# Performance work log

Measured on AMD Instinct MI355X. Metric: run time of the kernel, lower is better.

Reference implementation:

```python
import jax, jax.numpy as jnp
import numpy as np

D = 768        # d_model
F = 8192       # dict_size
N_UP = 3       # number of upstream autoencoders
K = 64         # topk
B, S = 2, 1024


def setup_inputs() -> dict:
    key = jax.random.key(0)
    ks = jax.random.split(key, 10)
    sc = 1.0 / np.sqrt(D)
    return {
        "feature_buffer": jnp.zeros((B, S, F), jnp.float32),
        "x": jax.random.normal(ks[0], (B, S, D), jnp.float32),
        "up_feats": jax.random.uniform(ks[1], (N_UP, B, S, F), jnp.float32),
        "W_enc": jax.random.normal(ks[2], (D, F), jnp.float32) * sc,
        "b_enc": jax.random.normal(ks[3], (F,), jnp.float32) * 0.01,
        "W_dec": jax.random.normal(ks[4], (F, D), jnp.float32) * sc,
        "b_dec": jax.random.normal(ks[5], (D,), jnp.float32) * 0.01,
        "up_W_dec": jax.random.normal(ks[6], (N_UP, F, D), jnp.float32) * sc,
        "up_b_dec": jax.random.normal(ks[7], (N_UP, D), jnp.float32) * 0.01,
        "conn_mask": jax.random.randint(ks[8], (N_UP, F, F), 0, 2).astype(bool),
        "k": K,
    }


def reference(feature_buffer, x, up_feats, W_enc, b_enc, W_dec, b_dec,
              up_W_dec, up_b_dec, conn_mask, k):
    # initial contribs: residual stream through current encoder
    approx = jnp.einsum("bsd,df->bsf", x, W_enc)            # [B,S,F]
    upstream_bias = jnp.zeros((D,), x.dtype)
    # accumulate pruned contributions from each upstream AE
    for i in range(up_feats.shape[0]):
        upstream_bias = upstream_bias + up_b_dec[i]
        # virtual weights up_dict -> down_dict, pruned by connection mask
        virt = (up_W_dec[i] @ W_enc) * conn_mask[i].astype(x.dtype)  # [F_up,F_down]
        approx = approx + jnp.einsum("bsf,fg->bsg", up_feats[i], virt)
    # bias correction: upstream decoder biases through encoder, plus encoder bias
    approx = approx + upstream_bias @ W_enc + b_enc          # [B,S,F]
    # topk + relu + scatter into the feature buffer
    top_vals, top_idx = jax.lax.top_k(approx, k)             # [B,S,k]
    top_vals = jax.nn.relu(top_vals)
    flat = feature_buffer.reshape(-1, F)
    rows = jnp.arange(flat.shape[0])[:, None]
    feat = flat.at[rows, top_idx.reshape(-1, k)].set(top_vals.reshape(-1, k))
    feat = feat.reshape(feature_buffer.shape)
    # decode
    return jnp.einsum("bsf,fd->bsd", feat, W_dec) + b_dec
```

## Files before the change

kernel.cpp:

```cpp
#include <hip/hip_runtime.h>
#include <hip/hip_bf16.h>


#define D_DIM 768
#define F_DIM 8192

typedef _Float16 f16;
typedef _Float16 f16x8 __attribute__((ext_vector_type(8)));
typedef float f32x4 __attribute__((ext_vector_type(4)));

#define BMN 128
#define BUFB 32768
#define PLNB 16384

__device__ inline void split_f32(float v, f16& h, f16& l) {
    float hf = (float)(f16)v;
    if (__builtin_fabsf(hf) < 6.1035156e-5f) hf = 0.f;
    h = (f16)hf;
    l = (f16)((v - hf) * 2048.0f);
}

template<int MODE>
__global__ __launch_bounds__(256, 2)
void mfma_gemm(const f16* __restrict__ Ap,
               const f16* __restrict__ Bp,
               float* __restrict__ C, int ldc,
               f16* __restrict__ Vp,
               const float* __restrict__ bias,
               const unsigned char* __restrict__ conn, int upIdx,
               const int* __restrict__ flagp,
               int K, int fdBase)
{
    __shared__ char lds[2 * BUFB];
    const int tid = threadIdx.x;
    const int bm = (MODE == 2 ? blockIdx.x : blockIdx.y) * BMN;
    const int bn = (MODE == 2 ? blockIdx.y : blockIdx.x) * BMN;

    const int w  = tid >> 6;
    const int l  = tid & 63;
    const int wr = (w >> 1) * 64;
    const int wc = (w & 1) * 64;

    const char* gsrc[8];
    #pragma unroll
    for (int j = 0; j < 8; ++j) {
        const int c = tid + 256 * j;
        const int p = c >> 10;
        const int q = c & 1023;
        const int r = q >> 3;
        const int sp = q & 7;
        const int slog = sp ^ (r & 7);
        const f16* base = p ? Bp : Ap;
        const int row0 = p ? bn : bm;
        gsrc[j] = (const char*)base + (size_t)(row0 + r) * ((size_t)K * 4)
                  + slog * 16;
    }

    #define STAGE(BUFSEL)                                                     \
        _Pragma("unroll")                                                     \
        for (int j = 0; j < 8; ++j) {                                         \
            __builtin_amdgcn_global_load_lds(                                 \
                (const __attribute__((address_space(1))) void*)gsrc[j],       \
                (__attribute__((address_space(3))) void*)                     \
                    (lds + (BUFSEL) * BUFB + (tid + 256 * j) * 16),           \
                16, 0, 0);                                                    \
            gsrc[j] += 128;                       \
        }

    f32x4 accH[4][4], accM[4][4];
    const f32x4 zero = {0.f, 0.f, 0.f, 0.f};
    #pragma unroll
    for (int a = 0; a < 4; ++a)
        #pragma unroll
        for (int b = 0; b < 4; ++b) { accH[a][b] = zero; accM[a][b] = zero; }

    const int steps = K >> 5;
    const int fr = l & 15;
    const int ks = l >> 4;

    int offAH[4], offBH[4], offAL[4], offBL[4];
    #pragma unroll
    for (int f = 0; f < 4; ++f) {
        const int ra = wr + f * 16 + fr;
        const int rb = wc + f * 16 + fr;
        offAH[f] = ra * 128 + ((ks ^ (ra & 7)) * 16);
        offAL[f] = ra * 128 + (((4 + ks) ^ (ra & 7)) * 16);
        offBH[f] = PLNB + rb * 128 + ((ks ^ (rb & 7)) * 16);
        offBL[f] = PLNB + rb * 128 + (((4 + ks) ^ (rb & 7)) * 16);
    }

    STAGE(0);
    int cur = 0;
    for (int t = 0; t < steps; ++t) {
        asm volatile("s_waitcnt vmcnt(0)" ::: "memory");
        __syncthreads();

        const char* Lb = lds + cur * BUFB;
        f16x8 ah[4], bh[4];
        #pragma unroll
        for (int mf = 0; mf < 4; ++mf) ah[mf] = *(const f16x8*)(Lb + offAH[mf]);
        #pragma unroll
        for (int nf = 0; nf < 4; ++nf) bh[nf] = *(const f16x8*)(Lb + offBH[nf]);

        if (t + 1 < steps) STAGE(cur ^ 1);

        f16x8 al[4], bl[4];
        #pragma unroll
        for (int nf = 0; nf < 4; ++nf) bl[nf] = *(const f16x8*)(Lb + offBL[nf]);
        #pragma unroll
        for (int mf = 0; mf < 4; ++mf) al[mf] = *(const f16x8*)(Lb + offAL[mf]);

        __builtin_amdgcn_s_setprio(1);
        #pragma unroll
        for (int nf = 0; nf < 4; ++nf)
            #pragma unroll
            for (int mf = 0; mf < 4; ++mf)
                accH[mf][nf] = __builtin_amdgcn_mfma_f32_16x16x32_f16(
                    ah[mf], bh[nf], accH[mf][nf], 0, 0, 0);
        __builtin_amdgcn_s_setprio(0);

        __builtin_amdgcn_s_setprio(1);
        #pragma unroll
        for (int nf = 0; nf < 4; ++nf)
            #pragma unroll
            for (int mf = 0; mf < 4; ++mf)
                accM[mf][nf] = __builtin_amdgcn_mfma_f32_16x16x32_f16(
                    ah[mf], bl[nf], accM[mf][nf], 0, 0, 0);
        #pragma unroll
        for (int mf = 0; mf < 4; ++mf)
            #pragma unroll
            for (int nf = 0; nf < 4; ++nf)
                accM[mf][nf] = __builtin_amdgcn_mfma_f32_16x16x32_f16(
                    al[mf], bh[nf], accM[mf][nf], 0, 0, 0);
        __builtin_amdgcn_s_setprio(0);

        cur ^= 1;
    }
    #undef STAGE

    const float MS = 4.8828125e-4f;
    const int flag = (MODE == 1) ? *flagp : 0;

    #pragma unroll
    for (int mf = 0; mf < 4; ++mf) {
        const int row0 = wr + mf * 16 + (l >> 4) * 4;
        #pragma unroll
        for (int nf = 0; nf < 4; ++nf) {
            const int col = wc + nf * 16 + (l & 15);
            float v[4];
            #pragma unroll
            for (int rr = 0; rr < 4; ++rr)
                v[rr] = accH[mf][nf][rr] + accM[mf][nf][rr] * MS;

            if (MODE == 0) {
                const float bb = bias[bn + col];
                #pragma unroll
                for (int rr = 0; rr < 4; ++rr)
                    C[(size_t)(bm + row0 + rr) * ldc + (bn + col)] = v[rr] + bb;
            } else if (MODE == 2) {
                #pragma unroll
                for (int rr = 0; rr < 4; ++rr) {
                    float* cp = &C[(size_t)(bm + row0 + rr) * ldc + (bn + col)];
                    *cp = *cp + v[rr];
                }
            } else {
                const size_t fu = (size_t)(bn + col);
                const size_t fd0 = (size_t)(fdBase + bm + row0);
                int m[4];
                if (flag == 1) {
                    const int4 mm = *(const int4*)((const int*)conn +
                        (size_t)upIdx * F_DIM * F_DIM + fu * F_DIM + fd0);
                    m[0] = mm.x; m[1] = mm.y; m[2] = mm.z; m[3] = mm.w;
                } else if (flag == 0) {
                    const uchar4 mm = *(const uchar4*)(conn +
                        (size_t)upIdx * F_DIM * F_DIM + fu * F_DIM + fd0);
                    m[0] = mm.x; m[1] = mm.y; m[2] = mm.z; m[3] = mm.w;
                } else if (flag == 2) {
                    const long long* pp = (const long long*)conn +
                        (size_t)upIdx * F_DIM * F_DIM + fu * F_DIM + fd0;
                    m[0] = (int)pp[0]; m[1] = (int)pp[1];
                    m[2] = (int)pp[2]; m[3] = (int)pp[3];
                } else {
                    const float4 mm = *(const float4*)((const float*)conn +
                        (size_t)upIdx * F_DIM * F_DIM + fu * F_DIM + fd0);
                    m[0] = mm.x != 0.f; m[1] = mm.y != 0.f;
                    m[2] = mm.z != 0.f; m[3] = mm.w != 0.f;
                }
                const size_t kblk = (fu >> 5) * 64 + (fu & 31);
                #pragma unroll
                for (int rr = 0; rr < 4; ++rr) {
                    const float vv = m[rr] ? v[rr] : 0.f;
                    f16 hh, ll;
                    split_f32(vv, hh, ll);
                    const size_t o = (size_t)(bm + row0 + rr) * (2 * F_DIM) + kblk;
                    Vp[o] = hh; Vp[o + 32] = ll;
                }
            }
        }
    }
}

__global__ __launch_bounds__(256)
void split_kernel(const float* __restrict__ src, f16* __restrict__ dst,
                  size_t n, int K)
{
    const size_t e = ((size_t)blockIdx.x * 256 + threadIdx.x) * 8;
    if (e >= n) return;
    const size_t r = e / (size_t)K;
    const int k = (int)(e - r * (size_t)K);
    const float4 a = *(const float4*)(src + e);
    const float4 b = *(const float4*)(src + e + 4);
    f16 hv[8], lv[8];
    const float s[8] = {a.x, a.y, a.z, a.w, b.x, b.y, b.z, b.w};
    #pragma unroll
    for (int i = 0; i < 8; ++i) split_f32(s[i], hv[i], lv[i]);
    const size_t base = r * (size_t)(2 * K) + (size_t)((k >> 5) * 64 + (k & 31));
    *(f16x8*)(dst + base)      = *(const f16x8*)hv;
    *(f16x8*)(dst + base + 32) = *(const f16x8*)lv;
}

__global__ __launch_bounds__(256)
void transpose_split_kernel(const float* __restrict__ W, f16* __restrict__ dst)
{
    const int f = blockIdx.x * 256 + threadIdx.x;
    for (int dc = 0; dc < D_DIM / 8; ++dc) {
        const int k = dc * 8;
        f16 hv[8], lv[8];
        #pragma unroll
        for (int j = 0; j < 8; ++j)
            split_f32(W[(size_t)(k + j) * F_DIM + f], hv[j], lv[j]);
        const size_t base = (size_t)f * (2 * D_DIM) + (k >> 5) * 64 + (k & 31);
        *(f16x8*)(dst + base)      = *(const f16x8*)hv;
        *(f16x8*)(dst + base + 32) = *(const f16x8*)lv;
    }
}

__global__ void detect_kernel(const int* __restrict__ conn, int* __restrict__ flag)
{
    __shared__ int not01, notf01, odd_nz;
    if (threadIdx.x == 0) { not01 = 0; notf01 = 0; odd_nz = 0; }
    __syncthreads();
    const int4 v = ((const int4*)conn)[threadIdx.x];
    const unsigned a[4] = {(unsigned)v.x, (unsigned)v.y,
                           (unsigned)v.z, (unsigned)v.w};
    int l_not01 = 0, l_notf = 0;
    #pragma unroll
    for (int i = 0; i < 4; ++i) {
        if (a[i] > 1u) l_not01 = 1;
        if (a[i] != 0u && a[i] != 0x3F800000u) l_notf = 1;
    }
    if (l_not01) atomicOr(&not01, 1);
    if (l_notf)  atomicOr(&notf01, 1);
    if (a[1] | a[3]) atomicOr(&odd_nz, 1);
    __syncthreads();
    if (threadIdx.x == 0) {
        int f;
        if (!not01)        f = odd_nz ? 1 : 2;
        else if (!notf01)  f = 3;
        else               f = 0;
        *flag = f;
    }
}

__global__ void bias2_kernel(const float* __restrict__ W_enc,
                             const float* __restrict__ b_enc,
                             const float* __restrict__ up_b_dec,
                             int nup, float* __restrict__ bias2)
{
    const int g = blockIdx.x * 256 + threadIdx.x;
    if (g >= F_DIM) return;
    float s = b_enc[g];
    for (int d = 0; d < D_DIM; ++d) {
        float ub = 0.f;
        for (int i = 0; i < nup; ++i) ub += up_b_dec[i * D_DIM + d];
        s = __builtin_fmaf(ub, W_enc[(size_t)d * F_DIM + g], s);
    }
    bias2[g] = s;
}

__global__ __launch_bounds__(256)
void topk_decode_kernel(const float* __restrict__ approx,
                        const float* __restrict__ W_dec,
                        const float* __restrict__ b_dec,
                        const int* __restrict__ kptr,
                        float* __restrict__ out)
{
    __shared__ unsigned keys[F_DIM];
    __shared__ int hist[256];
    __shared__ unsigned sh_prefix;
    __shared__ int sh_need;
    __shared__ int sel_cnt, eq_cnt;
    __shared__ int sidx[128];
    __shared__ float sval[128];
    __shared__ int eqidx[1024];

    const int tid = threadIdx.x;
    const int row = blockIdx.x;
    const int k = *kptr;
    const float* arow = approx + (size_t)row * F_DIM;

    for (int j = tid; j < F_DIM; j += 256) {
        unsigned u = __float_as_uint(arow[j]);
        u = (u & 0x80000000u) ? ~u : (u | 0x80000000u);
        keys[j] = u;
    }
    if (tid == 0) { sh_prefix = 0u; sh_need = k; sel_cnt = 0; eq_cnt = 0; }
    __syncthreads();

    for (int shift = 24; shift >= 0; shift -= 8) {
        if (tid < 256) hist[tid] = 0;
        __syncthreads();
        const unsigned pfx = sh_prefix;
        for (int j = tid; j < F_DIM; j += 256) {
            const unsigned u = keys[j];
            const bool match =
                (shift == 24) || ((u >> (shift + 8)) == (pfx >> (shift + 8)));
            if (match) atomicAdd(&hist[(u >> shift) & 255], 1);
        }
        __syncthreads();
        if (tid == 0) {
            int need = sh_need;
            for (int b = 255; b >= 0; --b) {
                const int c = hist[b];
                if (c >= need) {
                    sh_prefix = pfx | ((unsigned)b << shift);
                    sh_need = need;
                    break;
                }
                need -= c;
            }
        }
        __syncthreads();
    }
    const unsigned T = sh_prefix;
    const int r = sh_need;

    for (int j = tid; j < F_DIM; j += 256) {
        const unsigned u = keys[j];
        if (u > T) {
            const int p = atomicAdd(&sel_cnt, 1);
            sidx[p] = j;
        } else if (u == T) {
            const int p = atomicAdd(&eq_cnt, 1);
            if (p < 1024) eqidx[p] = j;
        }
    }
    __syncthreads();

    if (tid == 0) {
        const int m = sel_cnt;
        const int e = eq_cnt < 1024 ? eq_cnt : 1024;
        for (int t2 = 0; t2 < r; ++t2) {
            int best = 0x7FFFFFFF, bi = -1;
            for (int q = 0; q < e; ++q) {
                const int v = eqidx[q];
                if (v >= 0 && v < best) { best = v; bi = q; }
            }
            if (bi >= 0) { eqidx[bi] = -1; sidx[m + t2] = best; }
        }
        sel_cnt = m + r;
        const int n = sel_cnt;
        for (int a2 = 1; a2 < n; ++a2) {
            const int v = sidx[a2];
            int b2 = a2 - 1;
            while (b2 >= 0 && sidx[b2] > v) { sidx[b2 + 1] = sidx[b2]; --b2; }
            sidx[b2 + 1] = v;
        }
    }
    __syncthreads();

    const int total = sel_cnt;
    for (int j = tid; j < total; j += 256) {
        const float v = arow[sidx[j]];
        sval[j] = v > 0.f ? v : 0.f;
    }
    __syncthreads();

    float acc0 = b_dec[tid];
    float acc1 = b_dec[tid + 256];
    float acc2 = b_dec[tid + 512];
    for (int j = 0; j < total; ++j) {
        const float v = sval[j];
        const float* wv = W_dec + (size_t)sidx[j] * D_DIM;
        acc0 = __builtin_fmaf(v, wv[tid],       acc0);
        acc1 = __builtin_fmaf(v, wv[tid + 256], acc1);
        acc2 = __builtin_fmaf(v, wv[tid + 512], acc2);
    }
    float* orow = out + (size_t)row * D_DIM;
    orow[tid] = acc0;
    orow[tid + 256] = acc1;
    orow[tid + 512] = acc2;
}

extern "C" void kernel_launch(void* const* d_in, const int* in_sizes, int n_in,
                              void* d_out, int out_size, void* d_ws, size_t ws_size,
                              hipStream_t stream)
{
    const float* x         = (const float*)d_in[1];
    const float* up_feats  = (const float*)d_in[2];
    const float* W_enc     = (const float*)d_in[3];
    const float* b_enc     = (const float*)d_in[4];
    const float* W_dec     = (const float*)d_in[5];
    const float* b_dec     = (const float*)d_in[6];
    const float* up_W_dec  = (const float*)d_in[7];
    const float* up_b_dec  = (const float*)d_in[8];
    const unsigned char* conn = (const unsigned char*)d_in[9];
    const int* kptr        = (const int*)d_in[10];

    const int BS  = in_sizes[1] / D_DIM;
    const int NUP = in_sizes[8] / D_DIM;

    char* ws = (char*)d_ws;
    size_t off = 0;
    auto alloc = [&](size_t bytes) -> char* {
        off = (off + 255) & ~(size_t)255;
        char* p = ws + off; off += bytes; return p;
    };
    float* approx = (float*)alloc((size_t)BS * F_DIM * 4);
    float* bias2  = (float*)alloc(F_DIM * 4);
    int*   flag   = (int*)alloc(256);
    f16* xp   = (f16*)alloc((size_t)BS * D_DIM * 4);
    f16* Wtp  = (f16*)alloc((size_t)F_DIM * D_DIM * 4);
    f16* uwdp = (f16*)alloc((size_t)NUP * F_DIM * D_DIM * 4);
    f16* ufp  = (f16*)alloc((size_t)NUP * BS * F_DIM * 4);

    off = (off + 255) & ~(size_t)255;
    const size_t rem = (ws_size > off) ? ws_size - off : 0;
    int FC = (int)((rem / ((size_t)F_DIM * 4)) / 128 * 128);
    if (FC > F_DIM) FC = F_DIM;
    if (FC < 128) FC = 128;
    f16* vp = (f16*)alloc((size_t)FC * F_DIM * 4);

    detect_kernel<<<1, 256, 0, stream>>>((const int*)conn, flag);
    bias2_kernel<<<F_DIM / 256, 256, 0, stream>>>(W_enc, b_enc, up_b_dec, NUP, bias2);

    split_kernel<<<(unsigned)((size_t)BS * D_DIM / 2048), 256, 0, stream>>>(
        x, xp, (size_t)BS * D_DIM, D_DIM);
    split_kernel<<<(unsigned)((size_t)NUP * F_DIM * D_DIM / 2048), 256, 0, stream>>>(
        up_W_dec, uwdp, (size_t)NUP * F_DIM * D_DIM, D_DIM);
    split_kernel<<<(unsigned)((size_t)NUP * BS * F_DIM / 2048), 256, 0, stream>>>(
        up_feats, ufp, (size_t)NUP * BS * F_DIM, F_DIM);
    transpose_split_kernel<<<F_DIM / 256, 256, 0, stream>>>(W_enc, Wtp);

    mfma_gemm<0><<<dim3(F_DIM / BMN, BS / BMN), 256, 0, stream>>>(
        xp, Wtp, approx, F_DIM, nullptr, bias2,
        nullptr, 0, flag, D_DIM, 0);

    for (int i = 0; i < NUP; ++i) {
        for (int fc = 0; fc < F_DIM; fc += FC) {
            const int chunk = (F_DIM - fc) < FC ? (F_DIM - fc) : FC;
            mfma_gemm<1><<<dim3(F_DIM / BMN, chunk / BMN), 256, 0, stream>>>(
                Wtp + (size_t)fc * (2 * D_DIM),
                uwdp + (size_t)i * F_DIM * (2 * D_DIM),
                nullptr, 0, vp, nullptr,
                conn, i, flag, D_DIM, fc);
            mfma_gemm<2><<<dim3(BS / BMN, chunk / BMN), 256, 0, stream>>>(
                ufp + (size_t)i * BS * (2 * F_DIM),
                vp,
                approx + fc, F_DIM, nullptr, nullptr,
                nullptr, 0, flag, F_DIM, 0);
        }
    }

    topk_decode_kernel<<<BS, 256, 0, stream>>>(
        approx, W_dec, b_dec, kptr, (float*)d_out);
}
```

Baseline: 3.798 ms.

## Batch virtual-weight GEMMs and fuse all accumulation GEMMs into one segmented K loop

The per-upstream, per-chunk loop of virtual-weight and accumulation GEMM launches is replaced. One launch now computes the masked virtual weights for all upstream AEs, and a single segmented-K GEMM accumulates x·W_enc and the three up_feats·virt products in registers before writing approx once. This removes the repeated read-modify-write of approx and many kernel launches. In exchange it needs a full NUP×F×F split-f16 workspace (about 800 MB) instead of the workspace-sized chunking, and there is a risk of overrunning ws_size.

```diff
diff --git a/kernel.cpp b/kernel.cpp
--- a/kernel.cpp
+++ b/kernel.cpp
@@ -12,6 +12,14 @@
 #define BMN 128
 #define BUFB 32768
 #define PLNB 16384
+
+struct SegDesc {
+    const f16 *a0, *a1, *a2, *a3;
+    const f16 *b0, *b1, *b2, *b3;
+    int str0, str1, str2, str3;
+    int steps0, steps1, steps2, steps3;
+    int totalSteps;
+};
 
 __device__ inline void split_f32(float v, f16& h, f16& l) {
     float hf = (float)(f16)v;
@@ -22,39 +30,54 @@
 
 template<int MODE>
 __global__ __launch_bounds__(256, 2)
-void mfma_gemm(const f16* __restrict__ Ap,
-               const f16* __restrict__ Bp,
-               float* __restrict__ C, int ldc,
+void mfma_gemm(SegDesc d, float* __restrict__ C, int ldc,
                f16* __restrict__ Vp,
                const float* __restrict__ bias,
-               const unsigned char* __restrict__ conn, int upIdx,
-               const int* __restrict__ flagp,
-               int K, int fdBase)
+               const unsigned char* __restrict__ conn,
+               const int* __restrict__ flagp)
 {
     __shared__ char lds[2 * BUFB];
     const int tid = threadIdx.x;
-    const int bm = (MODE == 2 ? blockIdx.x : blockIdx.y) * BMN;
-    const int bn = (MODE == 2 ? blockIdx.y : blockIdx.x) * BMN;
+    int bm, bn, upIdx = 0;
+    if (MODE == 0) { bm = blockIdx.x * BMN; bn = blockIdx.y * BMN; }
+    else { upIdx = blockIdx.y >> 6; bm = (blockIdx.y & 63) * BMN;
+           bn = blockIdx.x * BMN; }
 
     const int w  = tid >> 6;
     const int l  = tid & 63;
     const int wr = (w >> 1) * 64;
     const int wc = (w & 1) * 64;
 
-    const char* gsrc[8];
+    int srow[8], soff[8], sisB[8];
     #pragma unroll
     for (int j = 0; j < 8; ++j) {
         const int c = tid + 256 * j;
-        const int p = c >> 10;
         const int q = c & 1023;
         const int r = q >> 3;
-        const int sp = q & 7;
-        const int slog = sp ^ (r & 7);
-        const f16* base = p ? Bp : Ap;
-        const int row0 = p ? bn : bm;
-        gsrc[j] = (const char*)base + (size_t)(row0 + r) * ((size_t)K * 4)
-                  + slog * 16;
-    }
+        sisB[j] = c >> 10;
+        srow[j] = r;
+        soff[j] = ((q & 7) ^ (r & 7)) * 16;
+    }
+
+    const char* gsrc[8];
+    auto computePtrs = [&](int seg) -> int {
+        const f16 *Ab, *Bb; int str, st;
+        switch (seg) {
+            case 0:  Ab = d.a0; Bb = d.b0; str = d.str0; st = d.steps0; break;
+            case 1:  Ab = d.a1; Bb = d.b1; str = d.str1; st = d.steps1; break;
+            case 2:  Ab = d.a2; Bb = d.b2; str = d.str2; st = d.steps2; break;
+            default: Ab = d.a3; Bb = d.b3; str = d.str3; st = d.steps3; break;
+        }
+        if (MODE == 1) Bb += (size_t)upIdx * F_DIM * 2 * D_DIM;
+        #pragma unroll
+        for (int j = 0; j < 8; ++j) {
+            const f16* base = sisB[j] ? Bb : Ab;
+            const int row0 = sisB[j] ? bn : bm;
+            gsrc[j] = (const char*)base
+                    + (size_t)(row0 + srow[j]) * (size_t)str + soff[j];
+        }
+        return st;
+    };
 
     #define STAGE(BUFSEL)                                                     \
         _Pragma("unroll")                                                     \
@@ -74,7 +97,6 @@
         #pragma unroll
         for (int b = 0; b < 4; ++b) { accH[a][b] = zero; accM[a][b] = zero; }
 
-    const int steps = K >> 5;
     const int fr = l & 15;
     const int ks = l >> 4;
 
@@ -89,9 +111,11 @@
         offBL[f] = PLNB + rb * 128 + (((4 + ks) ^ (rb & 7)) * 16);
     }
 
-    STAGE(0);
+    int seg = 0;
+    int rem = computePtrs(0);
+    STAGE(0); --rem;
     int cur = 0;
-    for (int t = 0; t < steps; ++t) {
+    for (int s = 0; s < d.totalSteps; ++s) {
         asm volatile("s_waitcnt vmcnt(0)" ::: "memory");
         __syncthreads();
 
@@ -102,7 +126,10 @@
         #pragma unroll
         for (int nf = 0; nf < 4; ++nf) bh[nf] = *(const f16x8*)(Lb + offBH[nf]);
 
-        if (t + 1 < steps) STAGE(cur ^ 1);
+        if (s + 1 < d.totalSteps) {
+            if (rem == 0) { ++seg; rem = computePtrs(seg); }
+            STAGE(cur ^ 1); --rem;
+        }
 
         f16x8 al[4], bl[4];
         #pragma unroll
@@ -140,6 +167,8 @@
 
     const float MS = 4.8828125e-4f;
     const int flag = (MODE == 1) ? *flagp : 0;
+    f16* Vq = (MODE == 1)
+        ? Vp + (size_t)upIdx * F_DIM * (2 * F_DIM) : nullptr;
 
     #pragma unroll
     for (int mf = 0; mf < 4; ++mf) {
@@ -157,15 +186,9 @@
                 #pragma unroll
                 for (int rr = 0; rr < 4; ++rr)
                     C[(size_t)(bm + row0 + rr) * ldc + (bn + col)] = v[rr] + bb;
-            } else if (MODE == 2) {
-                #pragma unroll
-                for (int rr = 0; rr < 4; ++rr) {
-                    float* cp = &C[(size_t)(bm + row0 + rr) * ldc + (bn + col)];
-                    *cp = *cp + v[rr];
-                }
             } else {
                 const size_t fu = (size_t)(bn + col);
-                const size_t fd0 = (size_t)(fdBase + bm + row0);
+                const size_t fd0 = (size_t)(bm + row0);
                 int m[4];
                 if (flag == 1) {
                     const int4 mm = *(const int4*)((const int*)conn +
@@ -193,7 +216,7 @@
                     f16 hh, ll;
                     split_f32(vv, hh, ll);
                     const size_t o = (size_t)(bm + row0 + rr) * (2 * F_DIM) + kblk;
-                    Vp[o] = hh; Vp[o + 32] = ll;
+                    Vq[o] = hh; Vq[o + 32] = ll;
                 }
             }
         }
@@ -423,13 +446,7 @@
     f16* Wtp  = (f16*)alloc((size_t)F_DIM * D_DIM * 4);
     f16* uwdp = (f16*)alloc((size_t)NUP * F_DIM * D_DIM * 4);
     f16* ufp  = (f16*)alloc((size_t)NUP * BS * F_DIM * 4);
-
-    off = (off + 255) & ~(size_t)255;
-    const size_t rem = (ws_size > off) ? ws_size - off : 0;
-    int FC = (int)((rem / ((size_t)F_DIM * 4)) / 128 * 128);
-    if (FC > F_DIM) FC = F_DIM;
-    if (FC < 128) FC = 128;
-    f16* vp = (f16*)alloc((size_t)FC * F_DIM * 4);
+    f16* vp   = (f16*)alloc((size_t)NUP * F_DIM * F_DIM * 4);
 
     detect_kernel<<<1, 256, 0, stream>>>((const int*)conn, flag);
     bias2_kernel<<<F_DIM / 256, 256, 0, stream>>>(W_enc, b_enc, up_b_dec, NUP, bias2);
@@ -442,24 +459,35 @@
         up_feats, ufp, (size_t)NUP * BS * F_DIM, F_DIM);
     transpose_split_kernel<<<F_DIM / 256, 256, 0, stream>>>(W_enc, Wtp);
 
-    mfma_gemm<0><<<dim3(F_DIM / BMN, BS / BMN), 256, 0, stream>>>(
-        xp, Wtp, approx, F_DIM, nullptr, bias2,
-        nullptr, 0, flag, D_DIM, 0);
-
-    for (int i = 0; i < NUP; ++i) {
-        for (int fc = 0; fc < F_DIM; fc += FC) {
-            const int chunk = (F_DIM - fc) < FC ? (F_DIM - fc) : FC;
-            mfma_gemm<1><<<dim3(F_DIM / BMN, chunk / BMN), 256, 0, stream>>>(
-                Wtp + (size_t)fc * (2 * D_DIM),
-                uwdp + (size_t)i * F_DIM * (2 * D_DIM),
-                nullptr, 0, vp, nullptr,
-                conn, i, flag, D_DIM, fc);
-            mfma_gemm<2><<<dim3(BS / BMN, chunk / BMN), 256, 0, stream>>>(
-                ufp + (size_t)i * BS * (2 * F_DIM),
-                vp,
-                approx + fc, F_DIM, nullptr, nullptr,
-                nullptr, 0, flag, F_DIM, 0);
-        }
+    {
+        SegDesc d1{};
+        d1.a0 = Wtp; d1.b0 = uwdp;
+        d1.str0 = D_DIM * 4; d1.steps0 = D_DIM / 32;
+        d1.totalSteps = D_DIM / 32;
+        mfma_gemm<1><<<dim3(F_DIM / BMN, (F_DIM / BMN) * NUP), 256, 0, stream>>>(
+            d1, nullptr, 0, vp, nullptr, conn, flag);
+    }
+
+    {
+        SegDesc d2{};
+        d2.a0 = xp;  d2.b0 = Wtp;
+        d2.str0 = D_DIM * 4; d2.steps0 = D_DIM / 32;
+        int total = D_DIM / 32;
+        const f16* aseg[3]; const f16* bseg[3]; 
+        for (int i = 0; i < NUP && i < 3; ++i) {
+            aseg[i] = ufp + (size_t)i * BS * 2 * F_DIM;
+            bseg[i] = vp  + (size_t)i * F_DIM * 2 * F_DIM;
+            total += F_DIM / 32;
+        }
+        if (NUP >= 1) { d2.a1 = aseg[0]; d2.b1 = bseg[0];
+                        d2.str1 = F_DIM * 4; d2.steps1 = F_DIM / 32; }
+        if (NUP >= 2) { d2.a2 = aseg[1]; d2.b2 = bseg[1];
+                        d2.str2 = F_DIM * 4; d2.steps2 = F_DIM / 32; }
+        if (NUP >= 3) { d2.a3 = aseg[2]; d2.b3 = bseg[2];
+                        d2.str3 = F_DIM * 4; d2.steps3 = F_DIM / 32; }
+        d2.totalSteps = total;
+        mfma_gemm<0><<<dim3(BS / BMN, F_DIM / BMN), 256, 0, stream>>>(
+            d2, approx, F_DIM, nullptr, bias2, nullptr, flag);
     }
 
     topk_decode_kernel<<<BS, 256, 0, stream>>>(
```

Result: faster. 3.621 ms (-4.6%).
